# Optimization experiments

Hardware: AMD Instinct MI355X
Metric: run time of the kernel (lower is better)

## Reference

```python
import jax, jax.numpy as jnp
import numpy as np
from jax import lax

# Config (matches init_kwargs)
E = 8         # num_routed_experts
K = 2         # topk
D = 2048      # d_model
H = 1408      # moe_hidden_dimension
NS = 2        # num_shared_experts
B, T = 2, 2048
EPS = 1e-20   # topk_norm_epsilon
HS = H * NS   # shared expert hidden dim


def setup_inputs() -> dict:
    key = jax.random.key(0)
    ks = jax.random.split(key, 8)
    s = 0.02
    return {
        "x": jax.random.normal(ks[0], (B, T, D), jnp.float32),
        "router_w": jax.random.normal(ks[1], (E, D), jnp.float32) * 0.006,
        # routed experts, stacked: gate/up: [E, D, H], down: [E, H, D]
        "wg": jax.random.normal(ks[2], (E, D, H), jnp.float32) * s,
        "wu": jax.random.normal(ks[3], (E, D, H), jnp.float32) * s,
        "wd": jax.random.normal(ks[4], (E, H, D), jnp.float32) * s,
        # shared expert (single big SwiGLU FFN)
        "sg": jax.random.normal(ks[5], (D, HS), jnp.float32) * s,
        "su": jax.random.normal(ks[6], (D, HS), jnp.float32) * s,
        "sd": jax.random.normal(ks[7], (HS, D), jnp.float32) * s,
    }


def _silu(v):
    return v * jax.nn.sigmoid(v)


def reference(x, router_w, wg, wu, wd, sg, su, sd):
    b, t, d = x.shape
    xf = x.reshape(b * t, d)                       # [N, D]
    n = xf.shape[0]

    # Router: softmax over experts, then top-k masking (DeepSeek style)
    gates = jax.nn.softmax(xf @ router_w.T, axis=-1)           # [N, E]
    topv, topi = lax.top_k(gates, K)                           # [N, K]
    masked = jnp.zeros_like(gates).at[jnp.arange(n)[:, None], topi].set(topv)
    # normalized_moe_gates=True
    masked = masked / (masked.sum(axis=-1, keepdims=True) + EPS)  # [N, E]

    # Per-expert SwiGLU FFN, weighted-accumulated over experts.
    # Mathematically identical to gather/grouped-GEMM/scatter-add combine:
    # tokens with zero gate for expert e contribute 0.
    def step(acc, p):
        wg_e, wu_e, wd_e, g_e = p                  # g_e: [N] gate weights
        y = (_silu(xf @ wg_e) * (xf @ wu_e)) @ wd_e  # [N, D]
        return acc + y * g_e[:, None], None

    routed, _ = lax.scan(step, jnp.zeros_like(xf), (wg, wu, wd, masked.T))

    # Shared experts (dense path applied to every token)
    shared = (_silu(xf @ sg) * (xf @ su)) @ sd      # [N, D]

    return (routed + shared).reshape(b, t, d)
```

## Files before the change

kernel.cpp:

```cpp
#include <hip/hip_runtime.h>
#include <hip/hip_bf16.h>
#include <cstdint>

#define NTOK 4096
#define DMODEL 2048
#define NEXP 8
#define HR 1408
#define HSHARED 2816
#define MAXT128 72

typedef __attribute__((ext_vector_type(8))) short bf16x8;
typedef __attribute__((ext_vector_type(4))) float f32x4;

__device__ inline unsigned short f2b(float f) {
    unsigned u = __float_as_uint(f);
    u += 0x7fffu + ((u >> 16) & 1u);
    return (unsigned short)(u >> 16);
}
__device__ inline unsigned pack2(float a, float b) {
    return (unsigned)f2b(a) | ((unsigned)f2b(b) << 16);
}

__device__ __forceinline__ void gll16(unsigned short* lds, const unsigned short* g) {
    __builtin_amdgcn_global_load_lds(
        (__attribute__((address_space(1))) void*)g,
        (__attribute__((address_space(3))) void*)lds, 16, 0, 0);
}

__global__ __launch_bounds__(256) void k_router2(const float* __restrict__ x,
                                                 const float* __restrict__ rw,
                                                 unsigned short* __restrict__ xb,
                                                 int* __restrict__ topi,
                                                 float* __restrict__ topw,
                                                 int* __restrict__ counts) {
    __shared__ float rws[NEXP * DMODEL];
    int tid = threadIdx.x;
    for (int i = tid * 4; i < NEXP * DMODEL; i += 1024)
        *(float4*)&rws[i] = *(const float4*)&rw[i];
    __syncthreads();
    int wv = tid >> 6, lane = tid & 63;
#pragma unroll
    for (int tk = 0; tk < 2; tk++) {
        int tok = blockIdx.x * 8 + wv * 2 + tk;
        const float* xr = x + (size_t)tok * DMODEL;
        unsigned short* xbr = xb + (size_t)tok * DMODEL;
        float s[NEXP] = {0.f,0.f,0.f,0.f,0.f,0.f,0.f,0.f};
#pragma unroll
        for (int i = 0; i < 8; i++) {
            int d = i * 256 + lane * 4;
            float4 xv = *(const float4*)(xr + d);
            uint2 p; p.x = pack2(xv.x, xv.y); p.y = pack2(xv.z, xv.w);
            *(uint2*)(xbr + d) = p;
#pragma unroll
            for (int e = 0; e < NEXP; e++) {
                float4 w = *(const float4*)&rws[e * DMODEL + d];
                s[e] = fmaf(xv.x, w.x, s[e]); s[e] = fmaf(xv.y, w.y, s[e]);
                s[e] = fmaf(xv.z, w.z, s[e]); s[e] = fmaf(xv.w, w.w, s[e]);
            }
        }
#pragma unroll
        for (int e = 0; e < NEXP; e++)
#pragma unroll
            for (int o = 32; o > 0; o >>= 1) s[e] += __shfl_xor(s[e], o, 64);
        if (lane == 0) {
            int i1 = 0;
#pragma unroll
            for (int e = 1; e < NEXP; e++) if (s[e] > s[i1]) i1 = e;
            int i2 = (i1 == 0) ? 1 : 0;
#pragma unroll
            for (int e = 0; e < NEXP; e++) if (e != i1 && s[e] > s[i2]) i2 = e;
            float mx = s[0];
#pragma unroll
            for (int e = 1; e < NEXP; e++) mx = fmaxf(mx, s[e]);
            float den = 0.f, ex[NEXP];
#pragma unroll
            for (int e = 0; e < NEXP; e++) { ex[e] = __expf(s[e] - mx); den += ex[e]; }
            float v1 = ex[i1] / den, v2 = ex[i2] / den;
            float inv = 1.f / (v1 + v2 + 1e-20f);
            topi[2 * tok] = i1; topi[2 * tok + 1] = i2;
            topw[2 * tok] = v1 * inv; topw[2 * tok + 1] = v2 * inv;
            atomicAdd(&counts[i1], 1); atomicAdd(&counts[i2], 1);
        }
    }
}

__global__ void k_scan(int* counts, int* offsets, int* cursors, int* ntiles,
                       int* tile_e, int* tile_r, int step) {
    if (threadIdx.x == 0 && blockIdx.x == 0) {
        int off = 0, nt = 0;
        for (int e = 0; e < NEXP; e++) {
            offsets[e] = off; cursors[e] = off;
            int c = counts[e];
            for (int r = 0; r < c; r += step) { tile_e[nt] = e; tile_r[nt] = r; nt++; }
            off += c;
        }
        ntiles[0] = nt;
    }
}

__global__ __launch_bounds__(256) void k_fill(const int* __restrict__ topi,
                                              const float* __restrict__ topw,
                                              int* cursors, int* at, float* aw) {
    int t = blockIdx.x * 256 + threadIdx.x;
    if (t >= NTOK) return;
#pragma unroll
    for (int k = 0; k < 2; k++) {
        int e = topi[2 * t + k];
        int pos = atomicAdd(&cursors[e], 1);
        at[pos] = t; aw[pos] = topw[2 * t + k];
    }
}

__device__ __forceinline__ void tcvt_tile(const float* __restrict__ src,
                                          unsigned short* __restrict__ dst,
                                          int N, int dstride, int n0, int k0) {
    __shared__ unsigned short T[64][72];
    int t = threadIdx.x;
    int kr = t >> 4, nc = (t & 15) * 4;
#pragma unroll
    for (int i = 0; i < 4; i++) {
        int k = kr + i * 16;
        float4 v = *(const float4*)(src + (size_t)(k0 + k) * N + n0 + nc);
        T[k][nc] = f2b(v.x); T[k][nc + 1] = f2b(v.y);
        T[k][nc + 2] = f2b(v.z); T[k][nc + 3] = f2b(v.w);
    }
    __syncthreads();
    int nr = t >> 3, kc = (t & 7) * 8;
#pragma unroll
    for (int j = 0; j < 2; j++) {
        int n = nr + j * 32;
        unsigned short tmp[8];
#pragma unroll
        for (int u = 0; u < 8; u++) tmp[u] = T[kc + u][n];
        *(uint4*)(dst + (size_t)(n0 + n) * dstride + k0 + kc) = *(uint4*)tmp;
    }
}

__global__ __launch_bounds__(256) void k_tcvt_gu(const float* __restrict__ wg,
                                                 const float* __restrict__ wu,
                                                 unsigned short* __restrict__ wgT,
                                                 unsigned short* __restrict__ wuT) {
    int z = blockIdx.z;
    const float* src = (z < 8 ? wg : wu) + (size_t)(z & 7) * DMODEL * HR;
    unsigned short* dst = (z < 8 ? wgT : wuT) + (size_t)(z & 7) * HR * DMODEL;
    tcvt_tile(src, dst, HR, DMODEL, blockIdx.x * 64, blockIdx.y * 64);
}

__global__ __launch_bounds__(256) void k_tcvt_s(const float* __restrict__ sg,
                                                const float* __restrict__ su,
                                                unsigned short* __restrict__ sgT,
                                                unsigned short* __restrict__ suT) {
    int z = blockIdx.z;
    tcvt_tile(z ? su : sg, z ? suT : sgT, HSHARED, DMODEL,
              blockIdx.x * 64, blockIdx.y * 64);
}

__global__ __launch_bounds__(256) void k_tcvt_d(const float* __restrict__ wd,
                                                const float* __restrict__ sd,
                                                unsigned short* __restrict__ wdT,
                                                unsigned short* __restrict__ sdT) {
    int z = blockIdx.z;
    const float* src;
    unsigned short* dst;
    int dstride;
    if (z < 8) {
        src = wd + (size_t)z * HR * DMODEL;
        dst = wdT + (size_t)z * DMODEL * HR;
        dstride = HR;
    } else {
        src = sd + (size_t)(z - 8) * HR * DMODEL;
        dst = sdT + (size_t)(z - 8) * HR;
        dstride = HSHARED;
    }
    tcvt_tile(src, dst, DMODEL, dstride, blockIdx.x * 64, blockIdx.y * 64);
}

#define GU_SH_JOBS 1408
#define GU_RT_NB   22
__global__ __launch_bounds__(256) void kg_all(
    const unsigned short* __restrict__ xb,
    const unsigned short* __restrict__ sgT, const unsigned short* __restrict__ suT,
    const unsigned short* __restrict__ wgT, const unsigned short* __restrict__ wuT,
    const int* __restrict__ tile_e, const int* __restrict__ tile_r,
    const int* __restrict__ offsets, const int* __restrict__ counts,
    const int* __restrict__ ntiles, const int* __restrict__ at,
    unsigned short* __restrict__ h_s, unsigned short* __restrict__ h_r) {
    int j = blockIdx.x;
    int m0, mcnt, n0, Hld;
    const unsigned short *Bg, *Bu;
    unsigned short* ho;
    bool gath;
    if (j < GU_SH_JOBS) {
        gath = false;
        m0 = (j / 44) * 128; mcnt = 128;
        n0 = (j % 44) * 64;
        Bg = sgT; Bu = suT; Hld = HSHARED; ho = h_s;
    } else {
        j -= GU_SH_JOBS;
        int tile = j / GU_RT_NB;
        if (tile >= ntiles[0]) return;
        gath = true;
        n0 = (j % GU_RT_NB) * 64;
        int e = tile_e[tile], ro = tile_r[tile];
        m0 = offsets[e] + ro;
        mcnt = counts[e] - ro; if (mcnt > 128) mcnt = 128;
        size_t wo = (size_t)e * HR * DMODEL;
        Bg = wgT + wo; Bu = wuT + wo; Hld = HR; ho = h_r;
    }

    __shared__ __align__(16) unsigned short As[128 * 64];
    __shared__ __align__(16) unsigned short Bgs[64 * 64];
    __shared__ __align__(16) unsigned short Bus[64 * 64];

    int tid = threadIdx.x;
    int wv = tid >> 6, lane = tid & 63;
    int rbase = tid >> 3;
    int kc = (tid & 7) ^ ((tid >> 3) & 7);
    const unsigned short* arp[4];
#pragma unroll
    for (int j2 = 0; j2 < 4; j2++) {
        int row = j2 * 32 + rbase;
        int cl = row < mcnt ? row : mcnt - 1;
        int grow = gath ? at[m0 + cl] : (m0 + cl);
        arp[j2] = xb + (size_t)grow * DMODEL + kc * 8;
    }
    const unsigned short* bgp[2];
    const unsigned short* bup[2];
#pragma unroll
    for (int j2 = 0; j2 < 2; j2++) {
        int row = j2 * 32 + rbase;
        bgp[j2] = Bg + (size_t)(n0 + row) * DMODEL + kc * 8;
        bup[j2] = Bu + (size_t)(n0 + row) * DMODEL + kc * 8;
    }
    unsigned short* a_l = As + (wv << 6) * 8;
    unsigned short* g_l = Bgs + (wv << 6) * 8;
    unsigned short* u_l = Bus + (wv << 6) * 8;

    int fr = lane & 15, quad = lane >> 4, sw = fr & 7;
    int wm = (wv & 1) << 6, wn = (wv >> 1) << 5;

    f32x4 accg[4][2] = {};
    f32x4 accu[4][2] = {};

    for (int k0 = 0; k0 < DMODEL; k0 += 64) {
        __syncthreads();
#pragma unroll
        for (int j2 = 0; j2 < 4; j2++) gll16(a_l + j2 * 2048, arp[j2] + k0);
#pragma unroll
        for (int j2 = 0; j2 < 2; j2++) {
            gll16(g_l + j2 * 2048, bgp[j2] + k0);
            gll16(u_l + j2 * 2048, bup[j2] + k0);
        }
        __syncthreads();
#pragma unroll
        for (int s = 0; s < 2; s++) {
            int off = (((s << 2) + quad) ^ sw) << 3;
            bf16x8 a[4], g[2], u[2];
#pragma unroll
            for (int tm = 0; tm < 4; tm++)
                a[tm] = *(const bf16x8*)&As[(wm + tm * 16 + fr) * 64 + off];
#pragma unroll
            for (int tn = 0; tn < 2; tn++) {
                int rb = (wn + tn * 16 + fr) * 64 + off;
                g[tn] = *(const bf16x8*)&Bgs[rb];
                u[tn] = *(const bf16x8*)&Bus[rb];
            }
#pragma unroll
            for (int tm = 0; tm < 4; tm++)
#pragma unroll
                for (int tn = 0; tn < 2; tn++) {
                    accg[tm][tn] = __builtin_amdgcn_mfma_f32_16x16x32_bf16(a[tm], g[tn], accg[tm][tn], 0, 0, 0);
                    accu[tm][tn] = __builtin_amdgcn_mfma_f32_16x16x32_bf16(a[tm], u[tn], accu[tm][tn], 0, 0, 0);
                }
        }
    }
#pragma unroll
    for (int tm = 0; tm < 4; tm++)
#pragma unroll
        for (int r = 0; r < 4; r++) {
            int row = wm + tm * 16 + (quad << 2) + r;
            if (row < mcnt) {
#pragma unroll
                for (int tn = 0; tn < 2; tn++) {
                    float gv = accg[tm][tn][r], uv = accu[tm][tn][r];
                    float hv = (gv / (1.f + __expf(-gv))) * uv;
                    ho[(size_t)(m0 + row) * Hld + n0 + wn + tn * 16 + fr] = f2b(hv);
                }
            }
        }
}

#define DN_SH_JOBS 512
__global__ __launch_bounds__(256) void kd_all(
    const unsigned short* __restrict__ h_s, const unsigned short* __restrict__ h_r,
    const unsigned short* __restrict__ sdT, const unsigned short* __restrict__ wdT,
    const int* __restrict__ tile_e, const int* __restrict__ tile_r,
    const int* __restrict__ offsets, const int* __restrict__ counts,
    const int* __restrict__ ntiles, const int* __restrict__ at,
    const float* __restrict__ aw, float* __restrict__ out) {
    int j = blockIdx.x;
    int m0, mcnt, n0, Kd;
    const unsigned short *Ab, *Bb;
    bool gath;
    if (j < DN_SH_JOBS) {
        gath = false;
        m0 = (j >> 4) * 128; mcnt = 128;
        n0 = (j & 15) * 128;
        Ab = h_s; Bb = sdT; Kd = HSHARED;
    } else {
        j -= DN_SH_JOBS;
        int tile = j >> 4;
        if (tile >= ntiles[0]) return;
        gath = true;
        n0 = (j & 15) * 128;
        int e = tile_e[tile], ro = tile_r[tile];
        m0 = offsets[e] + ro;
        mcnt = counts[e] - ro; if (mcnt > 128) mcnt = 128;
        Ab = h_r; Bb = wdT + (size_t)e * DMODEL * HR;
        Kd = HR;
    }

    __shared__ __align__(16) unsigned short As[128 * 64];
    __shared__ __align__(16) unsigned short Bs[128 * 64];

    int tid = threadIdx.x;
    int wv = tid >> 6, lane = tid & 63;
    int rbase = tid >> 3;
    int kc = (tid & 7) ^ ((tid >> 3) & 7);
    const unsigned short* arp[4];
    const unsigned short* brp[4];
#pragma unroll
    for (int j2 = 0; j2 < 4; j2++) {
        int row = j2 * 32 + rbase;
        int cl = row < mcnt ? row : mcnt - 1;
        arp[j2] = Ab + (size_t)(m0 + cl) * Kd + kc * 8;
        brp[j2] = Bb + (size_t)(n0 + row) * Kd + kc * 8;
    }
    unsigned short* a_l = As + (wv << 6) * 8;
    unsigned short* b_l = Bs + (wv << 6) * 8;

    int fr = lane & 15, quad = lane >> 4, sw = fr & 7;
    int wm = (wv & 1) << 6, wn = (wv >> 1) << 6;

    f32x4 acc[4][4] = {};

    for (int k0 = 0; k0 < Kd; k0 += 64) {
        __syncthreads();
#pragma unroll
        for (int j2 = 0; j2 < 4; j2++) {
            gll16(a_l + j2 * 2048, arp[j2] + k0);
            gll16(b_l + j2 * 2048, brp[j2] + k0);
        }
        __syncthreads();
#pragma unroll
        for (int s = 0; s < 2; s++) {
            int off = (((s << 2) + quad) ^ sw) << 3;
            bf16x8 a[4], b[4];
#pragma unroll
            for (int tm = 0; tm < 4; tm++)
                a[tm] = *(const bf16x8*)&As[(wm + tm * 16 + fr) * 64 + off];
#pragma unroll
            for (int tn = 0; tn < 4; tn++)
                b[tn] = *(const bf16x8*)&Bs[(wn + tn * 16 + fr) * 64 + off];
#pragma unroll
            for (int tm = 0; tm < 4; tm++)
#pragma unroll
                for (int tn = 0; tn < 4; tn++)
                    acc[tm][tn] = __builtin_amdgcn_mfma_f32_16x16x32_bf16(a[tm], b[tn], acc[tm][tn], 0, 0, 0);
        }
    }
#pragma unroll
    for (int tm = 0; tm < 4; tm++)
#pragma unroll
        for (int r = 0; r < 4; r++) {
            int row = wm + tm * 16 + (quad << 2) + r;
            if (row < mcnt) {
                int tok; float w;
                if (gath) { tok = at[m0 + row]; w = aw[m0 + row]; }
                else      { tok = m0 + row;     w = 1.f; }
#pragma unroll
                for (int tn = 0; tn < 4; tn++)
                    atomicAdd(&out[(size_t)tok * DMODEL + n0 + wn + tn * 16 + fr],
                              w * acc[tm][tn][r]);
            }
        }
}

template <bool GATHERED>
__global__ __launch_bounds__(256) void kf_gateup(
    const unsigned short* __restrict__ xb, const unsigned short* __restrict__ BgT,
    const unsigned short* __restrict__ BuT, int K, int Hld, int ebase,
    const int* __restrict__ tile_e, const int* __restrict__ tile_r,
    const int* __restrict__ offsets, const int* __restrict__ counts,
    const int* __restrict__ ntiles, const int* __restrict__ at,
    unsigned short* __restrict__ hout) {
    int m0, mcnt;
    const unsigned short* bgw = BgT;
    const unsigned short* buw = BuT;
    if (GATHERED) {
        if ((int)blockIdx.x >= ntiles[0]) return;
        int e = tile_e[blockIdx.x];
        if (e < ebase || e >= ebase + 4) return;
        int ro = tile_r[blockIdx.x];
        m0 = offsets[e] + ro;
        mcnt = counts[e] - ro; if (mcnt > 128) mcnt = 128;
        size_t wofs = (size_t)(e - ebase) * Hld * K;
        bgw += wofs; buw += wofs;
    } else { m0 = blockIdx.x * 128; mcnt = 128; }
    int n0 = blockIdx.y * 64;
    __shared__ __align__(16) unsigned short As[128 * 64];
    __shared__ __align__(16) unsigned short Bgs[64 * 64];
    __shared__ __align__(16) unsigned short Bus[64 * 64];
    int tid = threadIdx.x;
    int wv = tid >> 6, lane = tid & 63;
    int rbase = tid >> 3;
    int kc = (tid & 7) ^ ((tid >> 3) & 7);
    const unsigned short* arp[4];
#pragma unroll
    for (int j = 0; j < 4; j++) {
        int row = j * 32 + rbase;
        int cl = row < mcnt ? row : mcnt - 1;
        int grow = GATHERED ? at[m0 + cl] : (m0 + cl);
        arp[j] = xb + (size_t)grow * K + kc * 8;
    }
    const unsigned short* bgp[2];
    const unsigned short* bup[2];
#pragma unroll
    for (int j = 0; j < 2; j++) {
        int row = j * 32 + rbase;
        bgp[j] = bgw + (size_t)(n0 + row) * K + kc * 8;
        bup[j] = buw + (size_t)(n0 + row) * K + kc * 8;
    }
    unsigned short* a_l = As + (wv << 6) * 8;
    unsigned short* g_l = Bgs + (wv << 6) * 8;
    unsigned short* u_l = Bus + (wv << 6) * 8;
    int fr = lane & 15, quad = lane >> 4, sw = fr & 7;
    int wm = (wv & 1) << 6, wn = (wv >> 1) << 5;
    f32x4 accg[4][2] = {};
    f32x4 accu[4][2] = {};
    for (int k0 = 0; k0 < K; k0 += 64) {
        __syncthreads();
#pragma unroll
        for (int j = 0; j < 4; j++) gll16(a_l + j * 2048, arp[j] + k0);
#pragma unroll
        for (int j = 0; j < 2; j++) {
            gll16(g_l + j * 2048, bgp[j] + k0);
            gll16(u_l + j * 2048, bup[j] + k0);
        }
        __syncthreads();
#pragma unroll
        for (int s = 0; s < 2; s++) {
            int off = (((s << 2) + quad) ^ sw) << 3;
            bf16x8 a[4], g[2], u[2];
#pragma unroll
            for (int tm = 0; tm < 4; tm++)
                a[tm] = *(const bf16x8*)&As[(wm + tm * 16 + fr) * 64 + off];
#pragma unroll
            for (int tn = 0; tn < 2; tn++) {
                int rb = (wn + tn * 16 + fr) * 64 + off;
                g[tn] = *(const bf16x8*)&Bgs[rb];
                u[tn] = *(const bf16x8*)&Bus[rb];
            }
#pragma unroll
            for (int tm = 0; tm < 4; tm++)
#pragma unroll
                for (int tn = 0; tn < 2; tn++) {
                    accg[tm][tn] = __builtin_amdgcn_mfma_f32_16x16x32_bf16(a[tm], g[tn], accg[tm][tn], 0, 0, 0);
                    accu[tm][tn] = __builtin_amdgcn_mfma_f32_16x16x32_bf16(a[tm], u[tn], accu[tm][tn], 0, 0, 0);
                }
        }
    }
#pragma unroll
    for (int tm = 0; tm < 4; tm++)
#pragma unroll
        for (int r = 0; r < 4; r++) {
            int row = wm + tm * 16 + (quad << 2) + r;
            if (row < mcnt) {
#pragma unroll
                for (int tn = 0; tn < 2; tn++) {
                    float gv = accg[tm][tn][r], uv = accu[tm][tn][r];
                    float hv = (gv / (1.f + __expf(-gv))) * uv;
                    hout[(size_t)(m0 + row) * Hld + n0 + wn + tn * 16 + fr] = f2b(hv);
                }
            }
        }
}

template <bool GATHERED>
__global__ __launch_bounds__(256) void kf_down(
    const unsigned short* __restrict__ h, const unsigned short* __restrict__ BT,
    int K,
    const int* __restrict__ tile_e, const int* __restrict__ tile_r,
    const int* __restrict__ offsets, const int* __restrict__ counts,
    const int* __restrict__ ntiles, const int* __restrict__ at,
    const float* __restrict__ awt, float* __restrict__ out) {
    int m0, mcnt;
    const unsigned short* bw = BT;
    if (GATHERED) {
        if ((int)blockIdx.x >= ntiles[0]) return;
        int e = tile_e[blockIdx.x], ro = tile_r[blockIdx.x];
        m0 = offsets[e] + ro;
        mcnt = counts[e] - ro; if (mcnt > 128) mcnt = 128;
        bw += (size_t)e * DMODEL * K;
    } else { m0 = blockIdx.x * 128; mcnt = 128; }
    int n0 = blockIdx.y * 128;
    __shared__ __align__(16) unsigned short As[128 * 64];
    __shared__ __align__(16) unsigned short Bs[128 * 64];
    int tid = threadIdx.x;
    int wv = tid >> 6, lane = tid & 63;
    int rbase = tid >> 3;
    int kc = (tid & 7) ^ ((tid >> 3) & 7);
    const unsigned short* arp[4];
    const unsigned short* brp[4];
#pragma unroll
    for (int j = 0; j < 4; j++) {
        int row = j * 32 + rbase;
        int cl = row < mcnt ? row : mcnt - 1;
        arp[j] = h + (size_t)(m0 + cl) * K + kc * 8;
        brp[j] = bw + (size_t)(n0 + row) * K + kc * 8;
    }
    unsigned short* a_l = As + (wv << 6) * 8;
    unsigned short* b_l = Bs + (wv << 6) * 8;
    int fr = lane & 15, quad = lane >> 4, sw = fr & 7;
    int wm = (wv & 1) << 6, wn = (wv >> 1) << 6;
    f32x4 acc[4][4] = {};
    for (int k0 = 0; k0 < K; k0 += 64) {
        __syncthreads();
#pragma unroll
        for (int j = 0; j < 4; j++) {
            gll16(a_l + j * 2048, arp[j] + k0);
            gll16(b_l + j * 2048, brp[j] + k0);
        }
        __syncthreads();
#pragma unroll
        for (int s = 0; s < 2; s++) {
            int off = (((s << 2) + quad) ^ sw) << 3;
            bf16x8 a[4], b[4];
#pragma unroll
            for (int tm = 0; tm < 4; tm++)
                a[tm] = *(const bf16x8*)&As[(wm + tm * 16 + fr) * 64 + off];
#pragma unroll
            for (int tn = 0; tn < 4; tn++)
                b[tn] = *(const bf16x8*)&Bs[(wn + tn * 16 + fr) * 64 + off];
#pragma unroll
            for (int tm = 0; tm < 4; tm++)
#pragma unroll
                for (int tn = 0; tn < 4; tn++)
                    acc[tm][tn] = __builtin_amdgcn_mfma_f32_16x16x32_bf16(a[tm], b[tn], acc[tm][tn], 0, 0, 0);
        }
    }
#pragma unroll
    for (int tm = 0; tm < 4; tm++)
#pragma unroll
        for (int r = 0; r < 4; r++) {
            int row = wm + tm * 16 + (quad << 2) + r;
            if (row < mcnt) {
                if (GATHERED) {
                    int tok = at[m0 + row];
                    float w = awt[m0 + row];
#pragma unroll
                    for (int tn = 0; tn < 4; tn++)
                        atomicAdd(&out[(size_t)tok * DMODEL + n0 + wn + tn * 16 + fr],
                                  w * acc[tm][tn][r]);
                } else {
#pragma unroll
                    for (int tn = 0; tn < 4; tn++)
                        out[(size_t)(m0 + row) * DMODEL + n0 + wn + tn * 16 + fr] =
                            acc[tm][tn][r];
                }
            }
        }
}

__global__ __launch_bounds__(256) void k_tcvt(const float* __restrict__ src,
                                              unsigned short* __restrict__ dst,
                                              int K, int N) {
    src += (size_t)blockIdx.z * K * N;
    dst += (size_t)blockIdx.z * K * N;
    tcvt_tile(src, dst, N, K, blockIdx.x * 64, blockIdx.y * 64);
}

extern "C" void kernel_launch(void* const* d_in, const int* in_sizes, int n_in,
                              void* d_out, int out_size, void* d_ws, size_t ws_size,
                              hipStream_t stream) {
    (void)in_sizes; (void)n_in;
    const float* x  = (const float*)d_in[0];
    const float* rw = (const float*)d_in[1];
    const float* wg = (const float*)d_in[2];
    const float* wu = (const float*)d_in[3];
    const float* wd = (const float*)d_in[4];
    const float* sg = (const float*)d_in[5];
    const float* su = (const float*)d_in[6];
    const float* sd = (const float*)d_in[7];
    float* out = (float*)d_out;

    int* counts  = (int*)d_ws;
    int* offsets = counts + 8;
    int* cursors = counts + 16;
    int* ntiles  = counts + 24;
    int* tile_e  = counts + 32;
    int* tile_r  = tile_e + 144;
    int* topi    = tile_r + 144;
    float* topw  = (float*)(topi + 8192);
    int* at      = (int*)(topw + 8192);
    float* aw    = (float*)(at + 8192);

    const size_t META = 262144;
    const size_t XB   = (size_t)NTOK * DMODEL * 2;
    unsigned short* xb = (unsigned short*)((char*)d_ws + META);

    const size_t FULL_NEED = 178520064;
    const size_t FAST_NEED = 86245376;

    hipMemsetAsync(counts, 0, 32, stream);
    k_router2<<<dim3(512), 256, 0, stream>>>(x, rw, xb, topi, topw, counts);
    k_scan<<<1, 64, 0, stream>>>(counts, offsets, cursors, ntiles, tile_e, tile_r, 128);
    k_fill<<<dim3(NTOK / 256), 256, 0, stream>>>(topi, topw, cursors, at, aw);

    if (ws_size >= FULL_NEED) {
        char* pool = (char*)d_ws + META + XB;
        unsigned short* wgT = (unsigned short*)pool;
        unsigned short* wuT = (unsigned short*)(pool + 46137344);
        unsigned short* sgT = (unsigned short*)(pool + 92274688);
        unsigned short* suT = (unsigned short*)(pool + 103809024);
        unsigned short* wdT = (unsigned short*)pool;
        unsigned short* sdT = (unsigned short*)(pool + 46137344);
        unsigned short* h_r = (unsigned short*)(pool + 115343360);
        unsigned short* h_s = h_r + (size_t)8192 * HR;

        hipMemsetAsync(out, 0, (size_t)out_size * sizeof(float), stream);
        k_tcvt_gu<<<dim3(22, 32, 16), 256, 0, stream>>>(wg, wu, wgT, wuT);
        k_tcvt_s<<<dim3(44, 32, 2), 256, 0, stream>>>(sg, su, sgT, suT);
        kg_all<<<dim3(GU_SH_JOBS + MAXT128 * GU_RT_NB), 256, 0, stream>>>(
            xb, sgT, suT, wgT, wuT, tile_e, tile_r, offsets, counts, ntiles, at,
            h_s, h_r);
        k_tcvt_d<<<dim3(32, 22, 10), 256, 0, stream>>>(wd, sd, wdT, sdT);
        kd_all<<<dim3(DN_SH_JOBS + MAXT128 * 16), 256, 0, stream>>>(
            h_s, h_r, sdT, wdT, tile_e, tile_r, offsets, counts, ntiles, at, aw, out);
    } else {
        char* pool = (char*)d_ws + META + XB;
        unsigned short* sgT = (unsigned short*)pool;
        unsigned short* suT = (unsigned short*)(pool + 11534336);
        unsigned short* h_s = (unsigned short*)(pool + 23068672);
        unsigned short* sdT = (unsigned short*)(pool + 46137344);
        unsigned short* wgT = (unsigned short*)pool;
        unsigned short* wuT = (unsigned short*)(pool + 23068672);
        unsigned short* h_r = (unsigned short*)(pool + 46137344);
        unsigned short* wdT = (unsigned short*)pool;

        k_tcvt<<<dim3(HSHARED / 64, DMODEL / 64, 1), 256, 0, stream>>>(sg, sgT, DMODEL, HSHARED);
        k_tcvt<<<dim3(HSHARED / 64, DMODEL / 64, 1), 256, 0, stream>>>(su, suT, DMODEL, HSHARED);
        kf_gateup<false><<<dim3(NTOK / 128, HSHARED / 64), 256, 0, stream>>>(
            xb, sgT, suT, DMODEL, HSHARED, 0,
            nullptr, nullptr, nullptr, nullptr, nullptr, nullptr, h_s);
        k_tcvt<<<dim3(DMODEL / 64, HSHARED / 64, 1), 256, 0, stream>>>(sd, sdT, HSHARED, DMODEL);
        kf_down<false><<<dim3(NTOK / 128, DMODEL / 128), 256, 0, stream>>>(
            h_s, sdT, HSHARED,
            nullptr, nullptr, nullptr, nullptr, nullptr, nullptr, nullptr, out);
        k_tcvt<<<dim3(HR / 64, DMODEL / 64, 4), 256, 0, stream>>>(wg, wgT, DMODEL, HR);
        k_tcvt<<<dim3(HR / 64, DMODEL / 64, 4), 256, 0, stream>>>(wu, wuT, DMODEL, HR);
        kf_gateup<true><<<dim3(MAXT128, HR / 64), 256, 0, stream>>>(
            xb, wgT, wuT, DMODEL, HR, 0,
            tile_e, tile_r, offsets, counts, ntiles, at, h_r);
        k_tcvt<<<dim3(HR / 64, DMODEL / 64, 4), 256, 0, stream>>>(
            wg + (size_t)4 * DMODEL * HR, wgT, DMODEL, HR);
        k_tcvt<<<dim3(HR / 64, DMODEL / 64, 4), 256, 0, stream>>>(
            wu + (size_t)4 * DMODEL * HR, wuT, DMODEL, HR);
        kf_gateup<true><<<dim3(MAXT128, HR / 64), 256, 0, stream>>>(
            xb, wgT, wuT, DMODEL, HR, 4,
            tile_e, tile_r, offsets, counts, ntiles, at, h_r);
        k_tcvt<<<dim3(DMODEL / 64, HR / 64, 8), 256, 0, stream>>>(wd, wdT, HR, DMODEL);
        kf_down<true><<<dim3(MAXT128, DMODEL / 128), 256, 0, stream>>>(
            h_r, wdT, HR,
            tile_e, tile_r, offsets, counts, ntiles, at, aw, out);
    }
}
```

Measured before the change: 968.5 us.

## Fuse weight conversion into router and gate-up kernels to overlap with GEMMs

After: 989.5 us. 1.02x slower.

```diff
diff --git a/kernel.cpp b/kernel.cpp
--- a/kernel.cpp
+++ b/kernel.cpp
@@ -9,6 +9,13 @@
 #define HSHARED 2816
 #define MAXT128 72
 
+#define KG_SH 1408
+#define KG_TOTAL (KG_SH + 22 * MAXT128)
+#define CVT1_TOTAL 7040
+#define KD_GRID (512 + 16 * MAXT128)
+#define PREP_GRID (512 + 11264 + 2816)
+#define STRIPES 499
+
 typedef __attribute__((ext_vector_type(8))) short bf16x8;
 typedef __attribute__((ext_vector_type(4))) float f32x4;
 
@@ -27,21 +34,63 @@
         (__attribute__((address_space(3))) void*)lds, 16, 0, 0);
 }
 
-__global__ __launch_bounds__(256) void k_router2(const float* __restrict__ x,
-                                                 const float* __restrict__ rw,
-                                                 unsigned short* __restrict__ xb,
-                                                 int* __restrict__ topi,
-                                                 float* __restrict__ topw,
-                                                 int* __restrict__ counts) {
-    __shared__ float rws[NEXP * DMODEL];
+__device__ __forceinline__ void tcvt_tile(const float* __restrict__ src,
+                                          unsigned short* __restrict__ dst,
+                                          int N, int dstride, int n0, int k0,
+                                          unsigned short (*T)[72]) {
+    int t = threadIdx.x;
+    int kr = t >> 4, nc = (t & 15) * 4;
+#pragma unroll
+    for (int i = 0; i < 4; i++) {
+        int k = kr + i * 16;
+        float4 v = *(const float4*)(src + (size_t)(k0 + k) * N + n0 + nc);
+        T[k][nc] = f2b(v.x); T[k][nc + 1] = f2b(v.y);
+        T[k][nc + 2] = f2b(v.z); T[k][nc + 3] = f2b(v.w);
+    }
+    __syncthreads();
+    int nr = t >> 3, kc = (t & 7) * 8;
+#pragma unroll
+    for (int j = 0; j < 2; j++) {
+        int n = nr + j * 32;
+        unsigned short tmp[8];
+#pragma unroll
+        for (int u = 0; u < 8; u++) tmp[u] = T[kc + u][n];
+        *(uint4*)(dst + (size_t)(n0 + n) * dstride + k0 + kc) = *(uint4*)tmp;
+    }
+}
+
+__global__ __launch_bounds__(256) void k_prep(
+    const float* __restrict__ x, const float* __restrict__ rw,
+    const float* __restrict__ wg, const float* __restrict__ wu,
+    const float* __restrict__ sg, const float* __restrict__ su,
+    unsigned short* __restrict__ xb,
+    unsigned short* __restrict__ wgT, unsigned short* __restrict__ wuT,
+    unsigned short* __restrict__ sgT, unsigned short* __restrict__ suT,
+    int* __restrict__ topi, float* __restrict__ topw, int* __restrict__ counts) {
+    __shared__ unsigned short pT[64][72];
+    int bx = blockIdx.x;
+    if (bx >= 512) {
+        int t = bx - 512;
+        if (t < 11264) {
+            int z = t / 704, rem = t % 704;
+            int n_t = rem % 22, k_t = rem / 22;
+            const float* src = (z < 8 ? wg : wu) + (size_t)(z & 7) * DMODEL * HR;
+            unsigned short* dst = (z < 8 ? wgT : wuT) + (size_t)(z & 7) * HR * DMODEL;
+            tcvt_tile(src, dst, HR, DMODEL, n_t * 64, k_t * 64, pT);
+        } else {
+            int t2 = t - 11264;
+            int z = t2 / 1408, rem = t2 % 1408;
+            int n_t = rem % 44, k_t = rem / 44;
+            tcvt_tile(z ? su : sg, z ? suT : sgT, HSHARED, DMODEL,
+                      n_t * 64, k_t * 64, pT);
+        }
+        return;
+    }
     int tid = threadIdx.x;
-    for (int i = tid * 4; i < NEXP * DMODEL; i += 1024)
-        *(float4*)&rws[i] = *(const float4*)&rw[i];
-    __syncthreads();
     int wv = tid >> 6, lane = tid & 63;
 #pragma unroll
     for (int tk = 0; tk < 2; tk++) {
-        int tok = blockIdx.x * 8 + wv * 2 + tk;
+        int tok = bx * 8 + wv * 2 + tk;
         const float* xr = x + (size_t)tok * DMODEL;
         unsigned short* xbr = xb + (size_t)tok * DMODEL;
         float s[NEXP] = {0.f,0.f,0.f,0.f,0.f,0.f,0.f,0.f};
@@ -53,7 +102,7 @@
             *(uint2*)(xbr + d) = p;
 #pragma unroll
             for (int e = 0; e < NEXP; e++) {
-                float4 w = *(const float4*)&rws[e * DMODEL + d];
+                float4 w = *(const float4*)&rw[e * DMODEL + d];
                 s[e] = fmaf(xv.x, w.x, s[e]); s[e] = fmaf(xv.y, w.y, s[e]);
                 s[e] = fmaf(xv.z, w.z, s[e]); s[e] = fmaf(xv.w, w.w, s[e]);
             }
@@ -85,13 +134,13 @@
 }
 
 __global__ void k_scan(int* counts, int* offsets, int* cursors, int* ntiles,
-                       int* tile_e, int* tile_r, int step) {
+                       int* tile_e, int* tile_r) {
     if (threadIdx.x == 0 && blockIdx.x == 0) {
         int off = 0, nt = 0;
         for (int e = 0; e < NEXP; e++) {
             offsets[e] = off; cursors[e] = off;
             int c = counts[e];
-            for (int r = 0; r < c; r += step) { tile_e[nt] = e; tile_r[nt] = r; nt++; }
+            for (int r = 0; r < c; r += 128) { tile_e[nt] = e; tile_r[nt] = r; nt++; }
             off += c;
         }
         ntiles[0] = nt;
@@ -111,96 +160,61 @@
     }
 }
 
-__device__ __forceinline__ void tcvt_tile(const float* __restrict__ src,
-                                          unsigned short* __restrict__ dst,
-                                          int N, int dstride, int n0, int k0) {
-    __shared__ unsigned short T[64][72];
-    int t = threadIdx.x;
-    int kr = t >> 4, nc = (t & 15) * 4;
-#pragma unroll
-    for (int i = 0; i < 4; i++) {
-        int k = kr + i * 16;
-        float4 v = *(const float4*)(src + (size_t)(k0 + k) * N + n0 + nc);
-        T[k][nc] = f2b(v.x); T[k][nc + 1] = f2b(v.y);
-        T[k][nc + 2] = f2b(v.z); T[k][nc + 3] = f2b(v.w);
-    }
-    __syncthreads();
-    int nr = t >> 3, kc = (t & 7) * 8;
-#pragma unroll
-    for (int j = 0; j < 2; j++) {
-        int n = nr + j * 32;
-        unsigned short tmp[8];
-#pragma unroll
-        for (int u = 0; u < 8; u++) tmp[u] = T[kc + u][n];
-        *(uint4*)(dst + (size_t)(n0 + n) * dstride + k0 + kc) = *(uint4*)tmp;
-    }
-}
-
-__global__ __launch_bounds__(256) void k_tcvt_gu(const float* __restrict__ wg,
-                                                 const float* __restrict__ wu,
-                                                 unsigned short* __restrict__ wgT,
-                                                 unsigned short* __restrict__ wuT) {
-    int z = blockIdx.z;
-    const float* src = (z < 8 ? wg : wu) + (size_t)(z & 7) * DMODEL * HR;
-    unsigned short* dst = (z < 8 ? wgT : wuT) + (size_t)(z & 7) * HR * DMODEL;
-    tcvt_tile(src, dst, HR, DMODEL, blockIdx.x * 64, blockIdx.y * 64);
-}
-
-__global__ __launch_bounds__(256) void k_tcvt_s(const float* __restrict__ sg,
-                                                const float* __restrict__ su,
-                                                unsigned short* __restrict__ sgT,
-                                                unsigned short* __restrict__ suT) {
-    int z = blockIdx.z;
-    tcvt_tile(z ? su : sg, z ? suT : sgT, HSHARED, DMODEL,
-              blockIdx.x * 64, blockIdx.y * 64);
-}
-
-__global__ __launch_bounds__(256) void k_tcvt_d(const float* __restrict__ wd,
-                                                const float* __restrict__ sd,
-                                                unsigned short* __restrict__ wdT,
-                                                unsigned short* __restrict__ sdT) {
-    int z = blockIdx.z;
-    const float* src;
-    unsigned short* dst;
-    int dstride;
-    if (z < 8) {
-        src = wd + (size_t)z * HR * DMODEL;
-        dst = wdT + (size_t)z * DMODEL * HR;
-        dstride = HR;
-    } else {
-        src = sd + (size_t)(z - 8) * HR * DMODEL;
-        dst = sdT + (size_t)(z - 8) * HR;
-        dstride = HSHARED;
-    }
-    tcvt_tile(src, dst, DMODEL, dstride, blockIdx.x * 64, blockIdx.y * 64);
-}
-
-#define GU_SH_JOBS 1408
-#define GU_RT_NB   22
-__global__ __launch_bounds__(256) void kg_all(
+__global__ __launch_bounds__(256) void k_main1(
     const unsigned short* __restrict__ xb,
     const unsigned short* __restrict__ sgT, const unsigned short* __restrict__ suT,
     const unsigned short* __restrict__ wgT, const unsigned short* __restrict__ wuT,
+    const float* __restrict__ wd, const float* __restrict__ sd,
+    unsigned short* __restrict__ wdT, unsigned short* __restrict__ sdT,
     const int* __restrict__ tile_e, const int* __restrict__ tile_r,
     const int* __restrict__ offsets, const int* __restrict__ counts,
     const int* __restrict__ ntiles, const int* __restrict__ at,
-    unsigned short* __restrict__ h_s, unsigned short* __restrict__ h_r) {
-    int j = blockIdx.x;
+    unsigned short* __restrict__ h_s, unsigned short* __restrict__ h_r,
+    int kg_count, int cvt_count) {
+    __shared__ __align__(16) unsigned short smem[16384];
+    int bx = blockIdx.x;
+    int kgid = -1, cvid = -1;
+    if (cvt_count == 0) kgid = bx;
+    else if (kg_count == 0) cvid = bx;
+    else {
+        int s = bx / 21, r = bx % 21;
+        if (r < 6) { int id = s * 6 + r; if (id >= kg_count) return; kgid = id; }
+        else       { int id = s * 15 + (r - 6); if (id >= cvt_count) return; cvid = id; }
+    }
+
+    if (cvid >= 0) {
+        unsigned short (*T)[72] = (unsigned short(*)[72])smem;
+        if (cvid < 5632) {
+            int e = cvid / 704, rem = cvid % 704;
+            int n_t = rem % 32, k_t = rem / 32;
+            tcvt_tile(wd + (size_t)e * HR * DMODEL, wdT + (size_t)e * DMODEL * HR,
+                      DMODEL, HR, n_t * 64, k_t * 64, T);
+        } else {
+            int c2 = cvid - 5632;
+            int n_t = c2 % 32, k_t = c2 / 32;
+            tcvt_tile(sd, sdT, DMODEL, HSHARED, n_t * 64, k_t * 64, T);
+        }
+        return;
+    }
+
+    unsigned short* As = smem;
+    unsigned short* Bgs = smem + 8192;
+    unsigned short* Bus = smem + 12288;
     int m0, mcnt, n0, Hld;
     const unsigned short *Bg, *Bu;
     unsigned short* ho;
     bool gath;
-    if (j < GU_SH_JOBS) {
+    if (kgid < KG_SH) {
         gath = false;
-        m0 = (j / 44) * 128; mcnt = 128;
-        n0 = (j % 44) * 64;
+        n0 = (kgid >> 5) * 64;
+        m0 = (kgid & 31) * 128; mcnt = 128;
         Bg = sgT; Bu = suT; Hld = HSHARED; ho = h_s;
     } else {
-        j -= GU_SH_JOBS;
-        int tile = j / GU_RT_NB;
+        int id2 = kgid - KG_SH;
+        int tile = id2 % MAXT128;
         if (tile >= ntiles[0]) return;
         gath = true;
-        n0 = (j % GU_RT_NB) * 64;
+        n0 = (id2 / MAXT128) * 64;
         int e = tile_e[tile], ro = tile_r[tile];
         m0 = offsets[e] + ro;
         mcnt = counts[e] - ro; if (mcnt > 128) mcnt = 128;
@@ -208,29 +222,25 @@
         Bg = wgT + wo; Bu = wuT + wo; Hld = HR; ho = h_r;
     }
 
-    __shared__ __align__(16) unsigned short As[128 * 64];
-    __shared__ __align__(16) unsigned short Bgs[64 * 64];
-    __shared__ __align__(16) unsigned short Bus[64 * 64];
-
     int tid = threadIdx.x;
     int wv = tid >> 6, lane = tid & 63;
     int rbase = tid >> 3;
     int kc = (tid & 7) ^ ((tid >> 3) & 7);
     const unsigned short* arp[4];
 #pragma unroll
-    for (int j2 = 0; j2 < 4; j2++) {
-        int row = j2 * 32 + rbase;
+    for (int j = 0; j < 4; j++) {
+        int row = j * 32 + rbase;
         int cl = row < mcnt ? row : mcnt - 1;
         int grow = gath ? at[m0 + cl] : (m0 + cl);
-        arp[j2] = xb + (size_t)grow * DMODEL + kc * 8;
+        arp[j] = xb + (size_t)grow * DMODEL + kc * 8;
     }
     const unsigned short* bgp[2];
     const unsigned short* bup[2];
 #pragma unroll
-    for (int j2 = 0; j2 < 2; j2++) {
-        int row = j2 * 32 + rbase;
-        bgp[j2] = Bg + (size_t)(n0 + row) * DMODEL + kc * 8;
-        bup[j2] = Bu + (size_t)(n0 + row) * DMODEL + kc * 8;
+    for (int j = 0; j < 2; j++) {
+        int row = j * 32 + rbase;
+        bgp[j] = Bg + (size_t)(n0 + row) * DMODEL + kc * 8;
+        bup[j] = Bu + (size_t)(n0 + row) * DMODEL + kc * 8;
     }
     unsigned short* a_l = As + (wv << 6) * 8;
     unsigned short* g_l = Bgs + (wv << 6) * 8;
@@ -245,11 +255,11 @@
     for (int k0 = 0; k0 < DMODEL; k0 += 64) {
         __syncthreads();
 #pragma unroll
-        for (int j2 = 0; j2 < 4; j2++) gll16(a_l + j2 * 2048, arp[j2] + k0);
-#pragma unroll
-        for (int j2 = 0; j2 < 2; j2++) {
-            gll16(g_l + j2 * 2048, bgp[j2] + k0);
-            gll16(u_l + j2 * 2048, bup[j2] + k0);
+        for (int j = 0; j < 4; j++) gll16(a_l + j * 2048, arp[j] + k0);
+#pragma unroll
+        for (int j = 0; j < 2; j++) {
+            gll16(g_l + j * 2048, bgp[j] + k0);
+            gll16(u_l + j * 2048, bup[j] + k0);
         }
         __syncthreads();
 #pragma unroll
@@ -274,23 +284,30 @@
                 }
         }
     }
+    __syncthreads();
 #pragma unroll
     for (int tm = 0; tm < 4; tm++)
 #pragma unroll
         for (int r = 0; r < 4; r++) {
             int row = wm + tm * 16 + (quad << 2) + r;
-            if (row < mcnt) {
-#pragma unroll
-                for (int tn = 0; tn < 2; tn++) {
-                    float gv = accg[tm][tn][r], uv = accu[tm][tn][r];
-                    float hv = (gv / (1.f + __expf(-gv))) * uv;
-                    ho[(size_t)(m0 + row) * Hld + n0 + wn + tn * 16 + fr] = f2b(hv);
-                }
+#pragma unroll
+            for (int tn = 0; tn < 2; tn++) {
+                float gv = accg[tm][tn][r], uv = accu[tm][tn][r];
+                float hv = (gv / (1.f + __expf(-gv))) * uv;
+                smem[row * 72 + wn + tn * 16 + fr] = f2b(hv);
             }
         }
-}
-
-#define DN_SH_JOBS 512
+    __syncthreads();
+    int tr = tid >> 3, tc = (tid & 7) << 3;
+#pragma unroll
+    for (int i = 0; i < 4; i++) {
+        int row = i * 32 + tr;
+        if (row < mcnt)
+            *(uint4*)&ho[(size_t)(m0 + row) * Hld + n0 + tc] =
+                *(const uint4*)&smem[row * 72 + tc];
+    }
+}
+
 __global__ __launch_bounds__(256) void kd_all(
     const unsigned short* __restrict__ h_s, const unsigned short* __restrict__ h_r,
     const unsigned short* __restrict__ sdT, const unsigned short* __restrict__ wdT,
@@ -302,17 +319,17 @@
     int m0, mcnt, n0, Kd;
     const unsigned short *Ab, *Bb;
     bool gath;
-    if (j < DN_SH_JOBS) {
+    if (j < 512) {
         gath = false;
-        m0 = (j >> 4) * 128; mcnt = 128;
-        n0 = (j & 15) * 128;
+        n0 = (j >> 5) * 128;
+        m0 = (j & 31) * 128; mcnt = 128;
         Ab = h_s; Bb = sdT; Kd = HSHARED;
     } else {
-        j -= DN_SH_JOBS;
-        int tile = j >> 4;
+        int j2 = j - 512;
+        int tile = j2 % MAXT128;
         if (tile >= ntiles[0]) return;
         gath = true;
-        n0 = (j & 15) * 128;
+        n0 = (j2 / MAXT128) * 128;
         int e = tile_e[tile], ro = tile_r[tile];
         m0 = offsets[e] + ro;
         mcnt = counts[e] - ro; if (mcnt > 128) mcnt = 128;
@@ -384,200 +401,6 @@
                               w * acc[tm][tn][r]);
             }
         }
-}
-
-template <bool GATHERED>
-__global__ __launch_bounds__(256) void kf_gateup(
-    const unsigned short* __restrict__ xb, const unsigned short* __restrict__ BgT,
-    const unsigned short* __restrict__ BuT, int K, int Hld, int ebase,
-    const int* __restrict__ tile_e, const int* __restrict__ tile_r,
-    const int* __restrict__ offsets, const int* __restrict__ counts,
-    const int* __restrict__ ntiles, const int* __restrict__ at,
-    unsigned short* __restrict__ hout) {
-    int m0, mcnt;
-    const unsigned short* bgw = BgT;
-    const unsigned short* buw = BuT;
-    if (GATHERED) {
-        if ((int)blockIdx.x >= ntiles[0]) return;
-        int e = tile_e[blockIdx.x];
-        if (e < ebase || e >= ebase + 4) return;
-        int ro = tile_r[blockIdx.x];
-        m0 = offsets[e] + ro;
-        mcnt = counts[e] - ro; if (mcnt > 128) mcnt = 128;
-        size_t wofs = (size_t)(e - ebase) * Hld * K;
-        bgw += wofs; buw += wofs;
-    } else { m0 = blockIdx.x * 128; mcnt = 128; }
-    int n0 = blockIdx.y * 64;
-    __shared__ __align__(16) unsigned short As[128 * 64];
-    __shared__ __align__(16) unsigned short Bgs[64 * 64];
-    __shared__ __align__(16) unsigned short Bus[64 * 64];
-    int tid = threadIdx.x;
-    int wv = tid >> 6, lane = tid & 63;
-    int rbase = tid >> 3;
-    int kc = (tid & 7) ^ ((tid >> 3) & 7);
-    const unsigned short* arp[4];
-#pragma unroll
-    for (int j = 0; j < 4; j++) {
-        int row = j * 32 + rbase;
-        int cl = row < mcnt ? row : mcnt - 1;
-        int grow = GATHERED ? at[m0 + cl] : (m0 + cl);
-        arp[j] = xb + (size_t)grow * K + kc * 8;
-    }
-    const unsigned short* bgp[2];
-    const unsigned short* bup[2];
-#pragma unroll
-    for (int j = 0; j < 2; j++) {
-        int row = j * 32 + rbase;
-        bgp[j] = bgw + (size_t)(n0 + row) * K + kc * 8;
-        bup[j] = buw + (size_t)(n0 + row) * K + kc * 8;
-    }
-    unsigned short* a_l = As + (wv << 6) * 8;
-    unsigned short* g_l = Bgs + (wv << 6) * 8;
-    unsigned short* u_l = Bus + (wv << 6) * 8;
-    int fr = lane & 15, quad = lane >> 4, sw = fr & 7;
-    int wm = (wv & 1) << 6, wn = (wv >> 1) << 5;
-    f32x4 accg[4][2] = {};
-    f32x4 accu[4][2] = {};
-    for (int k0 = 0; k0 < K; k0 += 64) {
-        __syncthreads();
-#pragma unroll
-        for (int j = 0; j < 4; j++) gll16(a_l + j * 2048, arp[j] + k0);
-#pragma unroll
-        for (int j = 0; j < 2; j++) {
-            gll16(g_l + j * 2048, bgp[j] + k0);
-            gll16(u_l + j * 2048, bup[j] + k0);
-        }
-        __syncthreads();
-#pragma unroll
-        for (int s = 0; s < 2; s++) {
-            int off = (((s << 2) + quad) ^ sw) << 3;
-            bf16x8 a[4], g[2], u[2];
-#pragma unroll
-            for (int tm = 0; tm < 4; tm++)
-                a[tm] = *(const bf16x8*)&As[(wm + tm * 16 + fr) * 64 + off];
-#pragma unroll
-            for (int tn = 0; tn < 2; tn++) {
-                int rb = (wn + tn * 16 + fr) * 64 + off;
-                g[tn] = *(const bf16x8*)&Bgs[rb];
-                u[tn] = *(const bf16x8*)&Bus[rb];
-            }
-#pragma unroll
-            for (int tm = 0; tm < 4; tm++)
-#pragma unroll
-                for (int tn = 0; tn < 2; tn++) {
-                    accg[tm][tn] = __builtin_amdgcn_mfma_f32_16x16x32_bf16(a[tm], g[tn], accg[tm][tn], 0, 0, 0);
-                    accu[tm][tn] = __builtin_amdgcn_mfma_f32_16x16x32_bf16(a[tm], u[tn], accu[tm][tn], 0, 0, 0);
-                }
-        }
-    }
-#pragma unroll
-    for (int tm = 0; tm < 4; tm++)
-#pragma unroll
-        for (int r = 0; r < 4; r++) {
-            int row = wm + tm * 16 + (quad << 2) + r;
-            if (row < mcnt) {
-#pragma unroll
-                for (int tn = 0; tn < 2; tn++) {
-                    float gv = accg[tm][tn][r], uv = accu[tm][tn][r];
-                    float hv = (gv / (1.f + __expf(-gv))) * uv;
-                    hout[(size_t)(m0 + row) * Hld + n0 + wn + tn * 16 + fr] = f2b(hv);
-                }
-            }
-        }
-}
-
-template <bool GATHERED>
-__global__ __launch_bounds__(256) void kf_down(
-    const unsigned short* __restrict__ h, const unsigned short* __restrict__ BT,
-    int K,
-    const int* __restrict__ tile_e, const int* __restrict__ tile_r,
-    const int* __restrict__ offsets, const int* __restrict__ counts,
-    const int* __restrict__ ntiles, const int* __restrict__ at,
-    const float* __restrict__ awt, float* __restrict__ out) {
-    int m0, mcnt;
-    const unsigned short* bw = BT;
-    if (GATHERED) {
-        if ((int)blockIdx.x >= ntiles[0]) return;
-        int e = tile_e[blockIdx.x], ro = tile_r[blockIdx.x];
-        m0 = offsets[e] + ro;
-        mcnt = counts[e] - ro; if (mcnt > 128) mcnt = 128;
-        bw += (size_t)e * DMODEL * K;
-    } else { m0 = blockIdx.x * 128; mcnt = 128; }
-    int n0 = blockIdx.y * 128;
-    __shared__ __align__(16) unsigned short As[128 * 64];
-    __shared__ __align__(16) unsigned short Bs[128 * 64];
-    int tid = threadIdx.x;
-    int wv = tid >> 6, lane = tid & 63;
-    int rbase = tid >> 3;
-    int kc = (tid & 7) ^ ((tid >> 3) & 7);
-    const unsigned short* arp[4];
-    const unsigned short* brp[4];
-#pragma unroll
-    for (int j = 0; j < 4; j++) {
-        int row = j * 32 + rbase;
-        int cl = row < mcnt ? row : mcnt - 1;
-        arp[j] = h + (size_t)(m0 + cl) * K + kc * 8;
-        brp[j] = bw + (size_t)(n0 + row) * K + kc * 8;
-    }
-    unsigned short* a_l = As + (wv << 6) * 8;
-    unsigned short* b_l = Bs + (wv << 6) * 8;
-    int fr = lane & 15, quad = lane >> 4, sw = fr & 7;
-    int wm = (wv & 1) << 6, wn = (wv >> 1) << 6;
-    f32x4 acc[4][4] = {};
-    for (int k0 = 0; k0 < K; k0 += 64) {
-        __syncthreads();
-#pragma unroll
-        for (int j = 0; j < 4; j++) {
-            gll16(a_l + j * 2048, arp[j] + k0);
-            gll16(b_l + j * 2048, brp[j] + k0);
-        }
-        __syncthreads();
-#pragma unroll
-        for (int s = 0; s < 2; s++) {
-            int off = (((s << 2) + quad) ^ sw) << 3;
-            bf16x8 a[4], b[4];
-#pragma unroll
-            for (int tm = 0; tm < 4; tm++)
-                a[tm] = *(const bf16x8*)&As[(wm + tm * 16 + fr) * 64 + off];
-#pragma unroll
-            for (int tn = 0; tn < 4; tn++)
-                b[tn] = *(const bf16x8*)&Bs[(wn + tn * 16 + fr) * 64 + off];
-#pragma unroll
-            for (int tm = 0; tm < 4; tm++)
-#pragma unroll
-                for (int tn = 0; tn < 4; tn++)
-                    acc[tm][tn] = __builtin_amdgcn_mfma_f32_16x16x32_bf16(a[tm], b[tn], acc[tm][tn], 0, 0, 0);
-        }
-    }
-#pragma unroll
-    for (int tm = 0; tm < 4; tm++)
-#pragma unroll
-        for (int r = 0; r < 4; r++) {
-            int row = wm + tm * 16 + (quad << 2) + r;
-            if (row < mcnt) {
-                if (GATHERED) {
-                    int tok = at[m0 + row];
-                    float w = awt[m0 + row];
-#pragma unroll
-                    for (int tn = 0; tn < 4; tn++)
-                        atomicAdd(&out[(size_t)tok * DMODEL + n0 + wn + tn * 16 + fr],
-                                  w * acc[tm][tn][r]);
-                } else {
-#pragma unroll
-                    for (int tn = 0; tn < 4; tn++)
-                        out[(size_t)(m0 + row) * DMODEL + n0 + wn + tn * 16 + fr] =
-                            acc[tm][tn][r];
-                }
-            }
-        }
-}
-
-__global__ __launch_bounds__(256) void k_tcvt(const float* __restrict__ src,
-                                              unsigned short* __restrict__ dst,
-                                              int K, int N) {
-    src += (size_t)blockIdx.z * K * N;
-    dst += (size_t)blockIdx.z * K * N;
-    tcvt_tile(src, dst, N, K, blockIdx.x * 64, blockIdx.y * 64);
 }
 
 extern "C" void kernel_launch(void* const* d_in, const int* in_sizes, int n_in,
@@ -608,70 +431,51 @@
     const size_t META = 262144;
     const size_t XB   = (size_t)NTOK * DMODEL * 2;
     unsigned short* xb = (unsigned short*)((char*)d_ws + META);
-
-    const size_t FULL_NEED = 178520064;
-    const size_t FAST_NEED = 86245376;
+    char* pool = (char*)d_ws + META + XB;
+
+    const size_t SZ_WGT = 46137344;
+    const size_t SZ_SGT = 11534336;
+    const size_t SZ_H   = 23068672;
+    unsigned short* wgT = (unsigned short*)pool;
+    unsigned short* wuT = (unsigned short*)(pool + SZ_WGT);
+    unsigned short* sgT = (unsigned short*)(pool + 2 * SZ_WGT);
+    unsigned short* suT = (unsigned short*)(pool + 2 * SZ_WGT + SZ_SGT);
+    unsigned short* h_r = (unsigned short*)(pool + 2 * SZ_WGT + 2 * SZ_SGT);
+    unsigned short* h_s = (unsigned short*)(pool + 2 * SZ_WGT + 2 * SZ_SGT + SZ_H);
+
+    const size_t FULL2_NEED = META + XB + 2 * SZ_WGT + 2 * SZ_SGT + 2 * SZ_H
+                              + SZ_WGT + SZ_SGT;
+    bool full2 = ws_size >= FULL2_NEED;
+    unsigned short* wdT = full2
+        ? (unsigned short*)(pool + 2 * SZ_WGT + 2 * SZ_SGT + 2 * SZ_H)
+        : wgT;
+    unsigned short* sdT = full2
+        ? (unsigned short*)(pool + 2 * SZ_WGT + 2 * SZ_SGT + 2 * SZ_H + SZ_WGT)
+        : (unsigned short*)(pool + SZ_WGT);
 
     hipMemsetAsync(counts, 0, 32, stream);
-    k_router2<<<dim3(512), 256, 0, stream>>>(x, rw, xb, topi, topw, counts);
-    k_scan<<<1, 64, 0, stream>>>(counts, offsets, cursors, ntiles, tile_e, tile_r, 128);
+    hipMemsetAsync(out, 0, (size_t)out_size * sizeof(float), stream);
+
+    k_prep<<<dim3(PREP_GRID), 256, 0, stream>>>(
+        x, rw, wg, wu, sg, su, xb, wgT, wuT, sgT, suT, topi, topw, counts);
+    k_scan<<<1, 64, 0, stream>>>(counts, offsets, cursors, ntiles, tile_e, tile_r);
     k_fill<<<dim3(NTOK / 256), 256, 0, stream>>>(topi, topw, cursors, at, aw);
 
-    if (ws_size >= FULL_NEED) {
-        char* pool = (char*)d_ws + META + XB;
-        unsigned short* wgT = (unsigned short*)pool;
-        unsigned short* wuT = (unsigned short*)(pool + 46137344);
-        unsigned short* sgT = (unsigned short*)(pool + 92274688);
-        unsigned short* suT = (unsigned short*)(pool + 103809024);
-        unsigned short* wdT = (unsigned short*)pool;
-        unsigned short* sdT = (unsigned short*)(pool + 46137344);
-        unsigned short* h_r = (unsigned short*)(pool + 115343360);
-        unsigned short* h_s = h_r + (size_t)8192 * HR;
-
-        hipMemsetAsync(out, 0, (size_t)out_size * sizeof(float), stream);
-        k_tcvt_gu<<<dim3(22, 32, 16), 256, 0, stream>>>(wg, wu, wgT, wuT);
-        k_tcvt_s<<<dim3(44, 32, 2), 256, 0, stream>>>(sg, su, sgT, suT);
-        kg_all<<<dim3(GU_SH_JOBS + MAXT128 * GU_RT_NB), 256, 0, stream>>>(
-            xb, sgT, suT, wgT, wuT, tile_e, tile_r, offsets, counts, ntiles, at,
-            h_s, h_r);
-        k_tcvt_d<<<dim3(32, 22, 10), 256, 0, stream>>>(wd, sd, wdT, sdT);
-        kd_all<<<dim3(DN_SH_JOBS + MAXT128 * 16), 256, 0, stream>>>(
-            h_s, h_r, sdT, wdT, tile_e, tile_r, offsets, counts, ntiles, at, aw, out);
+    if (full2) {
+        k_main1<<<dim3(STRIPES * 21), 256, 0, stream>>>(
+            xb, sgT, suT, wgT, wuT, wd, sd, wdT, sdT,
+            tile_e, tile_r, offsets, counts, ntiles, at, h_s, h_r,
+            KG_TOTAL, CVT1_TOTAL);
     } else {
-        char* pool = (char*)d_ws + META + XB;
-        unsigned short* sgT = (unsigned short*)pool;
-        unsigned short* suT = (unsigned short*)(pool + 11534336);
-        unsigned short* h_s = (unsigned short*)(pool + 23068672);
-        unsigned short* sdT = (unsigned short*)(pool + 46137344);
-        unsigned short* wgT = (unsigned short*)pool;
-        unsigned short* wuT = (unsigned short*)(pool + 23068672);
-        unsigned short* h_r = (unsigned short*)(pool + 46137344);
-        unsigned short* wdT = (unsigned short*)pool;
-
-        k_tcvt<<<dim3(HSHARED / 64, DMODEL / 64, 1), 256, 0, stream>>>(sg, sgT, DMODEL, HSHARED);
-        k_tcvt<<<dim3(HSHARED / 64, DMODEL / 64, 1), 256, 0, stream>>>(su, suT, DMODEL, HSHARED);
-        kf_gateup<false><<<dim3(NTOK / 128, HSHARED / 64), 256, 0, stream>>>(
-            xb, sgT, suT, DMODEL, HSHARED, 0,
-            nullptr, nullptr, nullptr, nullptr, nullptr, nullptr, h_s);
-        k_tcvt<<<dim3(DMODEL / 64, HSHARED / 64, 1), 256, 0, stream>>>(sd, sdT, HSHARED, DMODEL);
-        kf_down<false><<<dim3(NTOK / 128, DMODEL / 128), 256, 0, stream>>>(
-            h_s, sdT, HSHARED,
-            nullptr, nullptr, nullptr, nullptr, nullptr, nullptr, nullptr, out);
-        k_tcvt<<<dim3(HR / 64, DMODEL / 64, 4), 256, 0, stream>>>(wg, wgT, DMODEL, HR);
-        k_tcvt<<<dim3(HR / 64, DMODEL / 64, 4), 256, 0, stream>>>(wu, wuT, DMODEL, HR);
-        kf_gateup<true><<<dim3(MAXT128, HR / 64), 256, 0, stream>>>(
-            xb, wgT, wuT, DMODEL, HR, 0,
-            tile_e, tile_r, offsets, counts, ntiles, at, h_r);
-        k_tcvt<<<dim3(HR / 64, DMODEL / 64, 4), 256, 0, stream>>>(
-            wg + (size_t)4 * DMODEL * HR, wgT, DMODEL, HR);
-        k_tcvt<<<dim3(HR / 64, DMODEL / 64, 4), 256, 0, stream>>>(
-            wu + (size_t)4 * DMODEL * HR, wuT, DMODEL, HR);
-        kf_gateup<true><<<dim3(MAXT128, HR / 64), 256, 0, stream>>>(
-            xb, wgT, wuT, DMODEL, HR, 4,
-            tile_e, tile_r, offsets, counts, ntiles, at, h_r);
-        k_tcvt<<<dim3(DMODEL / 64, HR / 64, 8), 256, 0, stream>>>(wd, wdT, HR, DMODEL);
-        kf_down<true><<<dim3(MAXT128, DMODEL / 128), 256, 0, stream>>>(
-            h_r, wdT, HR,
-            tile_e, tile_r, offsets, counts, ntiles, at, aw, out);
-    }
-}
+        k_main1<<<dim3(KG_TOTAL), 256, 0, stream>>>(
+            xb, sgT, suT, wgT, wuT, wd, sd, wdT, sdT,
+            tile_e, tile_r, offsets, counts, ntiles, at, h_s, h_r,
+            KG_TOTAL, 0);
+        k_main1<<<dim3(CVT1_TOTAL), 256, 0, stream>>>(
+            xb, sgT, suT, wgT, wuT, wd, sd, wdT, sdT,
+            tile_e, tile_r, offsets, counts, ntiles, at, h_s, h_r,
+            0, CVT1_TOTAL);
+    }
+    kd_all<<<dim3(KD_GRID), 256, 0, stream>>>(
+        h_s, h_r, sdT, wdT, tile_e, tile_r, offsets, counts, ntiles, at, aw, out);
+}
```
